# Optimization experiments

Measured on AMD Instinct MI355X. Metric: run time of the kernel, lower is better.

The kernel has to match this reference:

```python
import jax, jax.numpy as jnp
import numpy as np
from jax import lax

EPS = 1e-5
K = 3
PAD = 1
N_LAYERS = 7


def _conv2d(x, w, b):
    # x: [B,Cin,H,W], w: [Cout,Cin,K,K] -> [B,Cout,H,W], padding=1, stride=1
    y = lax.conv_general_dilated(x, w, window_strides=(1, 1),
                                 padding=[(PAD, PAD), (PAD, PAD)],
                                 dimension_numbers=('NCHW', 'OIHW', 'NCHW'))
    return y + b[None, :, None, None]


def _deform_conv2d(x, offset, weight):
    # torchvision deform_conv2d v1 (no mask, no bias), padding=PAD, stride=1.
    B, Cin, H, W = x.shape
    Cout = weight.shape[0]
    KK = K * K
    off = offset.reshape(B, KK, 2, H, W)
    dy = off[:, :, 0]  # [B,KK,H,W]
    dx = off[:, :, 1]
    kh = (jnp.arange(KK) // K).astype(x.dtype)  # row-major kernel taps
    kw = (jnp.arange(KK) % K).astype(x.dtype)
    hg = jnp.arange(H, dtype=x.dtype)
    wg = jnp.arange(W, dtype=x.dtype)
    # sampling positions p = p0 - pad + pk + offset
    py = dy + (hg[:, None] - PAD)[None, None, :, :] + kh[None, :, None, None]
    px = dx + (wg[None, :] - PAD)[None, None, :, :] + kw[None, :, None, None]
    y0 = jnp.floor(py)
    x0 = jnp.floor(px)
    ly = py - y0
    lx = px - x0
    y0i = y0.astype(jnp.int32)
    x0i = x0.astype(jnp.int32)

    def gather(img, yy, xx):  # img [Cin,H,W], yy/xx [KK,H,W]
        return img[:, yy, xx]  # [Cin,KK,H,W]

    gather_b = jax.vmap(gather)

    def corner(yi, xi, wgt):
        valid = (yi >= 0) & (yi < H) & (xi >= 0) & (xi < W)
        yc = jnp.clip(yi, 0, H - 1)
        xc = jnp.clip(xi, 0, W - 1)
        vals = gather_b(x, yc, xc)  # [B,Cin,KK,H,W]
        return vals * (wgt * valid)[:, None]

    sampled = (corner(y0i, x0i, (1 - ly) * (1 - lx))
               + corner(y0i, x0i + 1, (1 - ly) * lx)
               + corner(y0i + 1, x0i, ly * (1 - lx))
               + corner(y0i + 1, x0i + 1, ly * lx))  # [B,Cin,KK,H,W]
    return jnp.einsum('bikhw,oik->bohw', sampled, weight.reshape(Cout, Cin, KK))


def _layer(x, ow, ob, dw, g, b):
    offset = _conv2d(x, ow, ob)
    y = _deform_conv2d(x, offset, dw)
    # BatchNorm2d, training mode (batch stats, biased variance)
    mean = y.mean(axis=(0, 2, 3))
    var = y.var(axis=(0, 2, 3))
    yn = (y - mean[None, :, None, None]) * lax.rsqrt(var + EPS)[None, :, None, None]
    return jax.nn.relu(g[None, :, None, None] * yn + b[None, :, None, None])


def setup_inputs() -> dict:
    key = jax.random.key(0)
    ks = jax.random.split(key, 4)
    B, C, H, W = 4, 64, 128, 128
    x = jax.random.normal(ks[0], (B, C, H, W), dtype=jnp.float32)
    offset_w = jax.random.normal(ks[1], (N_LAYERS, 2 * K * K, C, K, K), dtype=jnp.float32) * 0.02
    offset_b = jnp.zeros((N_LAYERS, 2 * K * K), dtype=jnp.float32)
    deform_w = jax.random.normal(ks[2], (N_LAYERS, C, C, K, K), dtype=jnp.float32) * 0.05
    gamma = jnp.ones((N_LAYERS, C), dtype=jnp.float32)
    beta = jnp.zeros((N_LAYERS, C), dtype=jnp.float32)
    return {"x": x, "offset_w": offset_w, "offset_b": offset_b,
            "deform_w": deform_w, "gamma": gamma, "beta": beta}


def reference(x, offset_w, offset_b, deform_w, gamma, beta):
    def L(i, t):
        return _layer(t, offset_w[i], offset_b[i], deform_w[i], gamma[i], beta[i])
    # layer index map: 0=1_1, 1=1_2, 2=1_3, 3=1_4, 4=2_1, 5=2_2, 6=3
    out_1 = L(1, L(0, x))
    out_2 = L(4, x)
    out_sum_1 = out_1 + out_2
    out_1 = L(3, L(2, out_sum_1))
    out_2 = L(5, out_sum_1)
    out_3 = L(6, out_sum_1)
    return out_1 + out_2 + out_3
```

## Files before the change

kernel.cpp:

```cpp
#include <hip/hip_runtime.h>
#include <hip/hip_bf16.h>
#include <hip/hip_fp16.h>

#define NTOT 4194304
typedef __attribute__((ext_vector_type(4)))  short short4v;
typedef __attribute__((ext_vector_type(8)))  short short8v;
typedef __attribute__((ext_vector_type(4)))  float f32x4;
typedef __attribute__((ext_vector_type(2)))  float fx2;
typedef __attribute__((ext_vector_type(4)))  unsigned int uint4v;

__device__ __forceinline__ ushort f2bf(float f){
    __hip_bfloat16 h = __float2bfloat16(f);
    return __bfloat16_as_ushort(h);
}
__device__ __forceinline__ float bf2f(ushort u){
    return __uint_as_float(((unsigned)u)<<16);
}

__global__ __launch_bounds__(256) void pack_w(
    const float* __restrict__ dw, const float* __restrict__ ow,
    ushort* __restrict__ dwPk, ushort* __restrict__ owPk,
    float* __restrict__ statsG)
{
    int i = blockIdx.x*256 + threadIdx.x;
    if (i < 286720) {
        int j = i&3, co = (i>>2)&63, jg=(i>>8)&1, cih=(i>>9)&1, koff=(i>>10)&1;
        int r = i>>11; int kkp = r%5; int r2 = r/5; int ciq = r2&3; int l = r2>>2;
        int kk = kkp*2+koff, ci = ciq*16 + cih*8 + jg*4 + j;
        float v = (kk<9)? dw[((l*64+co)*64+ci)*9+kk] : 0.f;
        dwPk[i] = f2bf(v);
    }
    if (i < 143360) {
        int j = i&3, co = (i>>2)&31, jg=(i>>7)&1, cih=(i>>8)&1, koff=(i>>9)&1;
        int r = i>>10; int kkp = r%5; int r2 = r/5; int ciq = r2&3; int l = r2>>2;
        int kk = kkp*2+koff, ci = ciq*16 + cih*8 + jg*4 + j;
        float v = (kk<9 && co<18)? ow[((l*18+co)*64+ci)*9+kk] : 0.f;
        owPk[i] = f2bf(v);
    }
    if (i < 7*1024) statsG[i] = 0.f;
}

__global__ __launch_bounds__(256) void transpose_x(
    const float* __restrict__ src, ushort* __restrict__ xT)
{
    __shared__ ushort lds[128*72];
    const int bid = blockIdx.x, t = threadIdx.x;
    const int b = bid>>7, y = bid&127;
    const float* sp = src + (b<<20) + (y<<7);
#pragma unroll
    for (int i=0;i<32;i++){
        int lin = i*256 + t;
        int ci = lin>>7, xx = lin&127;
        lds[xx*72 + ci] = f2bf(sp[(ci<<14) + xx]);
    }
    __syncthreads();
    ushort* dp = xT + (((b<<7)+y)<<13);
#pragma unroll
    for (int i=0;i<4;i++){
        int u = i*256 + t;
        int xx = u>>3, cg = u&7;
        short8v v8 = *(const short8v*)(lds + xx*72 + cg*8);
        *(short8v*)(dp + (xx<<6) + cg*8) = v8;
    }
}

__constant__ int KHt[10] = {0,0,0,1,1,1,2,2,2,2};
__constant__ int KWt[10] = {0,1,2,0,1,2,0,1,2,2};

template<int NP>
__global__ __attribute__((amdgpu_flat_work_group_size(512,512), amdgpu_waves_per_eu(4,8)))
void dcn_layer(
    const ushort* __restrict__ xT, const ushort* __restrict__ owPkB,
    const float* __restrict__ obB, const ushort* __restrict__ dwPkB,
    ushort* __restrict__ ybB, float* __restrict__ statsB,
    int l0, int l1, int l2)
{
    constexpr int RS   = (NP==2)? 80 : 48;
    constexpr int UPP  = (NP==2)? 4  : 2;
    constexpr int SPS  = (NP==2)? 2  : 1;
    constexpr int CPP  = 4/NP;
    constexpr int TILE = 864*RS;
    constexpr int TOTU = 864*UPP;
    constexpr int ITER = (TOTU+511)/512;
    __shared__ __align__(16) char smem[TILE + 10240];
    __half* offh = (__half*)(smem + TILE);

    const int t = threadIdx.x, lane = t&63, w = t>>6;
    const int l15 = lane&15, lg = lane>>4;
    const int cih = lg&1, koff = lane>>5;
    const int bid = blockIdx.x;
    const int lsel = bid >> 8;
    const int tb = bid & 255;
    const int L = (lsel==0)? l0 : ((lsel==1)? l1 : l2);
    const ushort* owPk = owPkB + L*20480;
    const float*  ob   = obB   + L*18;
    const ushort* dwPk = dwPkB + L*40960;
    ushort* yb         = ybB + (size_t)lsel*NTOT;
    float*  statsL     = statsB + L*1024;

    const int xcd = tb&7, idx = tb>>3;
    const int b = xcd>>1, vh = xcd&1;
    const int ht = vh*8 + (idx>>2), wt = idx&3;
    const int w0 = wt*32, h0 = ht*8;
    const int row = h0 + w;
    const int RLO = h0-5, CLO = w0-8;
    const ushort* xb = xT + (b<<20);

    const short8v zz8 = (short8v){0,0,0,0,0,0,0,0};
    auto stage = [&](int P){
#pragma unroll 1
        for (int i=0;i<ITER;i++){
            int d = i*512 + t;
            if (d < TOTU) {
                int slot = d&(UPP-1), sp = d>>SPS;
                int rowt = sp/48, colt = sp - rowt*48;
                int gy = RLO+rowt, gx = CLO+colt;
                bool ok = ((unsigned)gy<128u) && ((unsigned)gx<128u);
                int gyc = min(max(gy,0),127), gxc = min(max(gx,0),127);
                short8v v = *(const short8v*)(xb + (((gyc<<7)+gxc)<<6) + (P*UPP+slot)*8);
                if (!ok) v = zz8;
                *(short8v*)(smem + sp*RS + ((slot^(sp&(UPP-1)))<<4)) = v;
            }
        }
    };

    f32x4 oacc[2][2];
#pragma unroll
    for (int p=0;p<2;p++)
#pragma unroll
        for (int q=0;q<2;q++) oacc[p][q] = (f32x4){0.f,0.f,0.f,0.f};

#pragma unroll 1
    for (int P=0; P<NP; ++P) {
        if (P) __syncthreads();
        stage(P);
        __syncthreads();
#pragma unroll 1
        for (int cil=0; cil<CPP; ++cil) {
            int ciq = P*CPP + cil;
            int unit = (NP==2)? ((cil<<1)|cih) : cih;
#pragma unroll 1
            for (int kkp=0; kkp<5; ++kkp) {
                int kkA = 2*kkp;
                int kkB = (kkA+1>8)?8:(kkA+1);
                int kh = koff ? KHt[kkB] : KHt[kkA];
                int kw = koff ? KWt[kkB] : KWt[kkA];
                short8v afr[2];
#pragma unroll
                for (int p=0;p<2;p++){
                    int rowt = w + kh + 4;
                    int colt = p*16 + l15 + kw + 7;
                    int sp = rowt*48 + colt;
                    afr[p] = *(const short8v*)(smem + sp*RS + ((unit^(sp&(UPP-1)))<<4));
                }
                const ushort* wop = owPk + ciq*5120 + kkp*1024 + koff*512 + cih*256;
#pragma unroll
                for (int q=0;q<2;q++){
                    short4v b0 = *(const short4v*)(wop +       (q*16+l15)*4);
                    short4v b1 = *(const short4v*)(wop + 128 + (q*16+l15)*4);
                    short8v bb = __builtin_shufflevector(b0,b1,0,1,2,3,4,5,6,7);
#pragma unroll
                    for (int p=0;p<2;p++)
                        oacc[p][q] = __builtin_amdgcn_mfma_f32_16x16x32_bf16(afr[p], bb, oacc[p][q], 0,0,0);
                }
            }
        }
    }

    {
        float biasq[2];
#pragma unroll
        for (int q=0;q<2;q++){ int o = q*16+l15; biasq[q] = (o<18)? ob[o] : 0.f; }
#pragma unroll
        for (int p=0;p<2;p++)
#pragma unroll
            for (int q=0;q<2;q++){
                int o = q*16+l15;
                if (o < 18) {
#pragma unroll
                    for (int r=0;r<4;r++){
                        int pix = w*32 + p*16 + lg*4 + r;
                        offh[pix*20 + o] = __float2half(oacc[p][q][r] + biasq[q]);
                    }
                }
            }
    }

    f32x4 acc[2][4];
#pragma unroll
    for (int p=0;p<2;p++)
#pragma unroll
        for (int q=0;q<4;q++) acc[p][q] = (f32x4){0.f,0.f,0.f,0.f};

#pragma unroll 1
    for (int P=0; P<NP; ++P) {
        __syncthreads();
        stage(P);
        __syncthreads();
#pragma unroll 1
        for (int cil=0; cil<CPP; ++cil) {
            int ciq = P*CPP + cil;
            int unit = (NP==2)? ((cil<<1)|cih) : cih;
#pragma unroll 1
            for (int kkp=0; kkp<5; ++kkp) {
                int kkA = 2*kkp;
                int kkB = (kkA+1>8)?8:(kkA+1);
                int kh = koff ? KHt[kkB] : KHt[kkA];
                int kw = koff ? KWt[kkB] : KWt[kkA];
                int kkX = koff ? kkB : kkA;
                short8v afr[2];
#pragma unroll
                for (int p=0;p<2;p++){
                    int pix = w*32 + p*16 + l15;
                    unsigned odp = *(const unsigned*)((const char*)offh + pix*40 + 4*kkX);
                    float dy = __half2float(__ushort_as_half((ushort)(odp & 0xffffu)));
                    float dx = __half2float(__ushort_as_half((ushort)(odp >> 16)));
                    float py = (float)(row + kh - 1) + dy;
                    float px = (float)(w0 + p*16 + l15 + kw - 1) + dx;
                    float fy = floorf(py), fx = floorf(px);
                    float ly = py - fy, lx = px - fx;
                    int y0 = (int)fy, x0 = (int)fx;
                    int y1 = y0+1, x1 = x0+1;
                    bool vy0 = ((unsigned)y0<128u), vy1 = ((unsigned)y1<128u);
                    bool vx0 = ((unsigned)x0<128u), vx1 = ((unsigned)x1<128u);
                    int y0c = min(max(y0,0),127), y1c = min(max(y1,0),127);
                    int x0c = min(max(x0,0),127), x1c = min(max(x1,0),127);
                    int r0 = y0c-RLO, r1 = y1c-RLO, c0 = x0c-CLO, c1 = x1c-CLO;
                    bool ty0 = ((unsigned)r0<18u), ty1 = ((unsigned)r1<18u);
                    bool tx0 = ((unsigned)c0<48u), tx1 = ((unsigned)c1<48u);
                    float g00 = (vy0&&vx0) ? (1.f-ly)*(1.f-lx) : 0.f;
                    float g01 = (vy0&&vx1) ? (1.f-ly)*lx       : 0.f;
                    float g10 = (vy1&&vx0) ? ly*(1.f-lx)       : 0.f;
                    float g11 = (vy1&&vx1) ? ly*lx             : 0.f;
                    float f00 = (ty0&&tx0) ? g00 : 0.f;
                    float f01 = (ty0&&tx1) ? g01 : 0.f;
                    float f10 = (ty1&&tx0) ? g10 : 0.f;
                    float f11 = (ty1&&tx1) ? g11 : 0.f;
                    int rc0 = min(max(r0,0),17), rc1 = min(max(r1,0),17);
                    int xc0 = min(max(c0,0),47), xc1 = min(max(c1,0),47);
                    int s00 = rc0*48+xc0, s01 = rc0*48+xc1, s10 = rc1*48+xc0, s11 = rc1*48+xc1;
                    uint4v q00 = *(const uint4v*)(smem + s00*RS + ((unit^(s00&(UPP-1)))<<4));
                    uint4v q01 = *(const uint4v*)(smem + s01*RS + ((unit^(s01&(UPP-1)))<<4));
                    uint4v q10 = *(const uint4v*)(smem + s10*RS + ((unit^(s10&(UPP-1)))<<4));
                    uint4v q11 = *(const uint4v*)(smem + s11*RS + ((unit^(s11&(UPP-1)))<<4));
                    fx2 F00 = {f00,f00}, F01 = {f01,f01}, F10 = {f10,f10}, F11 = {f11,f11};
                    fx2 sv2[4];
#pragma unroll
                    for (int k=0;k<4;k++){
                        fx2 xa = {__uint_as_float(q00[k]<<16), __uint_as_float(q00[k]&0xffff0000u)};
                        fx2 xb2= {__uint_as_float(q01[k]<<16), __uint_as_float(q01[k]&0xffff0000u)};
                        fx2 xc = {__uint_as_float(q10[k]<<16), __uint_as_float(q10[k]&0xffff0000u)};
                        fx2 xd = {__uint_as_float(q11[k]<<16), __uint_as_float(q11[k]&0xffff0000u)};
                        sv2[k] = xa*F00 + xb2*F01 + xc*F10 + xd*F11;
                    }
                    float r00 = g00-f00, r01 = g01-f01, r10 = g10-f10, r11 = g11-f11;
                    if (r00+r01+r10+r11 > 0.f) {
                        int cofs = (ciq*2 + cih)*8;
                        short8v a0 = *(const short8v*)(xb + ((((y0c<<7)+x0c)<<6) + cofs));
                        short8v a1 = *(const short8v*)(xb + ((((y0c<<7)+x1c)<<6) + cofs));
                        short8v a2 = *(const short8v*)(xb + ((((y1c<<7)+x0c)<<6) + cofs));
                        short8v a3 = *(const short8v*)(xb + ((((y1c<<7)+x1c)<<6) + cofs));
#pragma unroll
                        for (int j=0;j<8;j++){
                            float add = r00*bf2f((ushort)a0[j]) + r01*bf2f((ushort)a1[j])
                                      + r10*bf2f((ushort)a2[j]) + r11*bf2f((ushort)a3[j]);
                            if (j&1) sv2[j>>1].y += add; else sv2[j>>1].x += add;
                        }
                    }
#pragma unroll
                    for (int k=0;k<4;k++){
                        afr[p][2*k]   = (short)f2bf(sv2[k].x);
                        afr[p][2*k+1] = (short)f2bf(sv2[k].y);
                    }
                }
                const ushort* wp = dwPk + ciq*10240 + kkp*2048 + koff*1024 + cih*512;
#pragma unroll
                for (int q=0;q<4;q++){
                    short4v b0 = *(const short4v*)(wp +       (q*16+l15)*4);
                    short4v b1 = *(const short4v*)(wp + 256 + (q*16+l15)*4);
                    short8v bb = __builtin_shufflevector(b0,b1,0,1,2,3,4,5,6,7);
                    acc[0][q] = __builtin_amdgcn_mfma_f32_16x16x32_bf16(afr[0], bb, acc[0][q], 0,0,0);
                    acc[1][q] = __builtin_amdgcn_mfma_f32_16x16x32_bf16(afr[1], bb, acc[1][q], 0,0,0);
                }
            }
        }
    }

    float* yt  = (float*)smem;
    float* red = (float*)(smem + 33280);
#pragma unroll
    for (int half=0; half<2; ++half){
        __syncthreads();
#pragma unroll
        for (int p=0;p<2;p++)
#pragma unroll
            for (int qq=0;qq<2;qq++)
                *(f32x4*)(yt + (qq*16+l15)*260 + w*32 + p*16 + lg*4) = acc[p][half*2+qq];
        __syncthreads();
#pragma unroll
        for (int i=0;i<2;i++){
            int u = i*512 + t;
            int co = u>>5, px8 = (u&31)*8;
            short8v v8;
#pragma unroll
            for (int e=0;e<8;e++) v8[e] = (short)f2bf(yt[co*260 + px8 + e]);
            *(short8v*)(yb + ((((b<<6) + half*32 + co)<<14)
                        + ((h0 + (px8>>5))<<7) + w0 + (px8&31))) = v8;
        }
        {
            float s=0.f, s2=0.f;
            int co = t&31, seg = t>>5;
            const float* bp = yt + co*260 + seg*16;
#pragma unroll
            for (int qd=0;qd<16;qd++){ float v = bp[qd]; s += v; s2 += v*v; }
            red[seg*32+co] = s; red[512 + seg*32+co] = s2;
        }
        __syncthreads();
        if (t < 64){
            int vv = t>>5, cc = t&31;
            float a = 0.f;
#pragma unroll
            for (int g=0;g<16;g++) a += red[vv*512 + g*32 + cc];
            atomicAdd(statsL + (tb&7)*128 + vv*64 + half*32 + cc, a);
        }
    }
}

__global__ __launch_bounds__(256) void norm_fuse(
    const ushort* __restrict__ yv, const float* __restrict__ statsL,
    const float* __restrict__ gamma, const float* __restrict__ beta,
    const ushort* __restrict__ addB, float* __restrict__ dstF,
    ushort* __restrict__ dstB, ushort* __restrict__ xTout, int mode)
{
    __shared__ float scs[64], shs[64];
    __shared__ ushort lt[128*72];
    const int bid = blockIdx.x, t = threadIdx.x;
    const int b = bid>>7, y = bid&127;
    if (t < 64){
        float sum=0.f, ssq=0.f;
#pragma unroll
        for (int s=0;s<8;s++){ sum += statsL[s*128+t]; ssq += statsL[s*128+64+t]; }
        float mean = sum*(1.f/65536.f);
        float var  = ssq*(1.f/65536.f) - mean*mean;
        float inv  = rsqrtf(var + 1e-5f);
        float sc = gamma[t]*inv;
        scs[t] = sc; shs[t] = beta[t] - mean*sc;
    }
    __syncthreads();
#pragma unroll
    for (int i=0;i<4;i++){
        int g = i*256 + t;
        int ch = g>>4, xg = (g&15)*8;
        long base = (long)(((b<<6)+ch)<<14) + (y<<7) + xg;
        short8v v8 = *(const short8v*)(yv + base);
        float sc = scs[ch], sh = shs[ch];
        float r[8];
#pragma unroll
        for (int e=0;e<8;e++) r[e] = fmaxf(bf2f((ushort)v8[e])*sc+sh, 0.f);
        if (mode & 2) {
            short8v a8 = *(const short8v*)(addB + base);
#pragma unroll
            for (int e=0;e<8;e++) r[e] += bf2f((ushort)a8[e]);
        }
        if (mode & 4) {
            const float4* op = (const float4*)(dstF + base);
            float4 a0 = op[0], a1 = op[1];
            r[0]+=a0.x; r[1]+=a0.y; r[2]+=a0.z; r[3]+=a0.w;
            r[4]+=a1.x; r[5]+=a1.y; r[6]+=a1.z; r[7]+=a1.w;
        }
        if (mode & 5) {
            float4* dp = (float4*)(dstF + base);
            dp[0] = make_float4(r[0],r[1],r[2],r[3]);
            dp[1] = make_float4(r[4],r[5],r[6],r[7]);
        }
        if (mode & 16) {
            short8v o8;
#pragma unroll
            for (int e=0;e<8;e++) o8[e] = (short)f2bf(r[e]);
            *(short8v*)(dstB + base) = o8;
        }
        if (mode & 8) {
#pragma unroll
            for (int e=0;e<8;e++) lt[(xg+e)*72 + ch] = f2bf(r[e]);
        }
    }
    if (mode & 8) {
        __syncthreads();
        ushort* dp = xTout + (((b<<7)+y)<<13);
#pragma unroll
        for (int i=0;i<4;i++){
            int u = i*256 + t;
            int xx = u>>3, cg = u&7;
            short8v v8 = *(const short8v*)(lt + xx*72 + cg*8);
            *(short8v*)(dp + (xx<<6) + cg*8) = v8;
        }
    }
}

extern "C" void kernel_launch(void* const* d_in, const int* in_sizes, int n_in,
                              void* d_out, int out_size, void* d_ws, size_t ws_size,
                              hipStream_t stream)
{
    const float* x  = (const float*)d_in[0];
    const float* ow = (const float*)d_in[1];
    const float* ob = (const float*)d_in[2];
    const float* dw = (const float*)d_in[3];
    const float* g  = (const float*)d_in[4];
    const float* be = (const float*)d_in[5];
    float* out = (float*)d_out;

    ushort* yb     = (ushort*)d_ws;
    ushort* t4b    = yb + 3*(size_t)NTOT;
    ushort* xA     = t4b + NTOT;
    ushort* xB     = xA + NTOT;
    float*  statsG = (float*)(xB + NTOT);
    ushort* dwPk   = (ushort*)(statsG + 7*1024);
    ushort* owPk   = dwPk + 286720;

    pack_w<<<1120, 256, 0, stream>>>(dw, ow, dwPk, owPk, statsG);
    transpose_x<<<512, 256, 0, stream>>>(x, xA);

    auto nf = [&](int l, const ushort* ybp, int mode, const ushort* addB,
                  float* dstF, ushort* dstB, ushort* xout){
        norm_fuse<<<512, 256, 0, stream>>>(ybp, statsG + l*1024, g + l*64, be + l*64,
                                           addB, dstF, dstB, xout, mode);
    };

    dcn_layer<2><<<512, 512, 0, stream>>>(xA, owPk, ob, dwPk, yb, statsG, 4, 0, 4);
    nf(4, yb,        16, nullptr, nullptr, t4b,    nullptr);
    nf(0, yb+NTOT,    8, nullptr, nullptr, nullptr, xB);
    dcn_layer<2><<<256, 512, 0, stream>>>(xB, owPk, ob, dwPk, yb, statsG, 1, 1, 1);
    nf(1, yb,        10, t4b,    nullptr, nullptr, xA);
    dcn_layer<4><<<768, 512, 0, stream>>>(xA, owPk, ob, dwPk, yb, statsG, 2, 5, 6);
    nf(2, yb,         8, nullptr, nullptr, nullptr, xB);
    nf(5, yb+NTOT,    1, nullptr, out,     nullptr, nullptr);
    nf(6, yb+2*(size_t)NTOT, 5, nullptr, out, nullptr, nullptr);
    dcn_layer<2><<<256, 512, 0, stream>>>(xB, owPk, ob, dwPk, yb, statsG, 3, 3, 3);
    nf(3, yb,         5, nullptr, out,     nullptr, nullptr);
}
```

Before: 318.0 us.

## Pair layer 6 with layer 3 launch and drop NP=4 variant, simplify fallback

Removes the NP=4 template path and pairs layers differently: layer 2 runs with layer 5, and layer 6 now launches together with layer 3, reading a second input tensor. Each launch is 512 blocks using the larger tile layout. The bilinear gather drops the global-bounds clamp in the common path and takes the slow global-memory fallback only when a tap falls outside the staged tile but inside the image. This rebalances grid sizes across launches, removes the large 768-block launch, and trims per-sample ALU work. It also cuts the workspace to two y buffers. Layer 6's normalization moves to the end, and since both layers of the final launch now write through the two y buffers, correctness depends on that buffer indexing.

```diff
diff --git a/kernel.cpp b/kernel.cpp
--- a/kernel.cpp
+++ b/kernel.cpp
@@ -67,23 +67,15 @@
 __constant__ int KHt[10] = {0,0,0,1,1,1,2,2,2,2};
 __constant__ int KWt[10] = {0,1,2,0,1,2,0,1,2,2};
 
-template<int NP>
 __global__ __attribute__((amdgpu_flat_work_group_size(512,512), amdgpu_waves_per_eu(4,8)))
 void dcn_layer(
-    const ushort* __restrict__ xT, const ushort* __restrict__ owPkB,
-    const float* __restrict__ obB, const ushort* __restrict__ dwPkB,
-    ushort* __restrict__ ybB, float* __restrict__ statsB,
-    int l0, int l1, int l2)
+    const ushort* __restrict__ xTA, const ushort* __restrict__ xTB,
+    const ushort* __restrict__ owPkB, const float* __restrict__ obB,
+    const ushort* __restrict__ dwPkB, ushort* __restrict__ ybB,
+    float* __restrict__ statsB, int l0, int l1)
 {
-    constexpr int RS   = (NP==2)? 80 : 48;
-    constexpr int UPP  = (NP==2)? 4  : 2;
-    constexpr int SPS  = (NP==2)? 2  : 1;
-    constexpr int CPP  = 4/NP;
-    constexpr int TILE = 864*RS;
-    constexpr int TOTU = 864*UPP;
-    constexpr int ITER = (TOTU+511)/512;
-    __shared__ __align__(16) char smem[TILE + 10240];
-    __half* offh = (__half*)(smem + TILE);
+    __shared__ __align__(16) char smem[79360];
+    __half* offh = (__half*)(smem + 69120);
 
     const int t = threadIdx.x, lane = t&63, w = t>>6;
     const int l15 = lane&15, lg = lane>>4;
@@ -91,7 +83,7 @@
     const int bid = blockIdx.x;
     const int lsel = bid >> 8;
     const int tb = bid & 255;
-    const int L = (lsel==0)? l0 : ((lsel==1)? l1 : l2);
+    const int L = lsel ? l1 : l0;
     const ushort* owPk = owPkB + L*20480;
     const float*  ob   = obB   + L*18;
     const ushort* dwPk = dwPkB + L*40960;
@@ -104,22 +96,22 @@
     const int w0 = wt*32, h0 = ht*8;
     const int row = h0 + w;
     const int RLO = h0-5, CLO = w0-8;
-    const ushort* xb = xT + (b<<20);
+    const ushort* xb = (lsel ? xTB : xTA) + (b<<20);
 
     const short8v zz8 = (short8v){0,0,0,0,0,0,0,0};
     auto stage = [&](int P){
 #pragma unroll 1
-        for (int i=0;i<ITER;i++){
+        for (int i=0;i<7;i++){
             int d = i*512 + t;
-            if (d < TOTU) {
-                int slot = d&(UPP-1), sp = d>>SPS;
+            if (d < 3456) {
+                int slot = d&3, sp = d>>2;
                 int rowt = sp/48, colt = sp - rowt*48;
                 int gy = RLO+rowt, gx = CLO+colt;
                 bool ok = ((unsigned)gy<128u) && ((unsigned)gx<128u);
                 int gyc = min(max(gy,0),127), gxc = min(max(gx,0),127);
-                short8v v = *(const short8v*)(xb + (((gyc<<7)+gxc)<<6) + (P*UPP+slot)*8);
+                short8v v = *(const short8v*)(xb + (((gyc<<7)+gxc)<<6) + (P*4+slot)*8);
                 if (!ok) v = zz8;
-                *(short8v*)(smem + sp*RS + ((slot^(sp&(UPP-1)))<<4)) = v;
+                *(short8v*)(smem + sp*80 + ((slot^(sp&3))<<4)) = v;
             }
         }
     };
@@ -131,14 +123,14 @@
         for (int q=0;q<2;q++) oacc[p][q] = (f32x4){0.f,0.f,0.f,0.f};
 
 #pragma unroll 1
-    for (int P=0; P<NP; ++P) {
+    for (int P=0; P<2; ++P) {
         if (P) __syncthreads();
         stage(P);
         __syncthreads();
 #pragma unroll 1
-        for (int cil=0; cil<CPP; ++cil) {
-            int ciq = P*CPP + cil;
-            int unit = (NP==2)? ((cil<<1)|cih) : cih;
+        for (int cil=0; cil<2; ++cil) {
+            int ciq = P*2 + cil;
+            int unit = (cil<<1)|cih;
 #pragma unroll 1
             for (int kkp=0; kkp<5; ++kkp) {
                 int kkA = 2*kkp;
@@ -151,7 +143,7 @@
                     int rowt = w + kh + 4;
                     int colt = p*16 + l15 + kw + 7;
                     int sp = rowt*48 + colt;
-                    afr[p] = *(const short8v*)(smem + sp*RS + ((unit^(sp&(UPP-1)))<<4));
+                    afr[p] = *(const short8v*)(smem + sp*80 + ((unit^(sp&3))<<4));
                 }
                 const ushort* wop = owPk + ciq*5120 + kkp*1024 + koff*512 + cih*256;
 #pragma unroll
@@ -193,14 +185,14 @@
         for (int q=0;q<4;q++) acc[p][q] = (f32x4){0.f,0.f,0.f,0.f};
 
 #pragma unroll 1
-    for (int P=0; P<NP; ++P) {
+    for (int P=0; P<2; ++P) {
         __syncthreads();
         stage(P);
         __syncthreads();
 #pragma unroll 1
-        for (int cil=0; cil<CPP; ++cil) {
-            int ciq = P*CPP + cil;
-            int unit = (NP==2)? ((cil<<1)|cih) : cih;
+        for (int cil=0; cil<2; ++cil) {
+            int ciq = P*2 + cil;
+            int unit = (cil<<1)|cih;
 #pragma unroll 1
             for (int kkp=0; kkp<5; ++kkp) {
                 int kkA = 2*kkp;
@@ -220,29 +212,23 @@
                     float fy = floorf(py), fx = floorf(px);
                     float ly = py - fy, lx = px - fx;
                     int y0 = (int)fy, x0 = (int)fx;
-                    int y1 = y0+1, x1 = x0+1;
-                    bool vy0 = ((unsigned)y0<128u), vy1 = ((unsigned)y1<128u);
-                    bool vx0 = ((unsigned)x0<128u), vx1 = ((unsigned)x1<128u);
-                    int y0c = min(max(y0,0),127), y1c = min(max(y1,0),127);
-                    int x0c = min(max(x0,0),127), x1c = min(max(x1,0),127);
-                    int r0 = y0c-RLO, r1 = y1c-RLO, c0 = x0c-CLO, c1 = x1c-CLO;
+                    int r0 = y0 - RLO, c0 = x0 - CLO;
+                    int r1 = r0 + 1,  c1 = c0 + 1;
                     bool ty0 = ((unsigned)r0<18u), ty1 = ((unsigned)r1<18u);
                     bool tx0 = ((unsigned)c0<48u), tx1 = ((unsigned)c1<48u);
-                    float g00 = (vy0&&vx0) ? (1.f-ly)*(1.f-lx) : 0.f;
-                    float g01 = (vy0&&vx1) ? (1.f-ly)*lx       : 0.f;
-                    float g10 = (vy1&&vx0) ? ly*(1.f-lx)       : 0.f;
-                    float g11 = (vy1&&vx1) ? ly*lx             : 0.f;
-                    float f00 = (ty0&&tx0) ? g00 : 0.f;
-                    float f01 = (ty0&&tx1) ? g01 : 0.f;
-                    float f10 = (ty1&&tx0) ? g10 : 0.f;
-                    float f11 = (ty1&&tx1) ? g11 : 0.f;
+                    float w00 = (1.f-ly)*(1.f-lx), w01 = (1.f-ly)*lx;
+                    float w10 = ly*(1.f-lx),       w11 = ly*lx;
+                    float f00 = (ty0&&tx0)? w00 : 0.f;
+                    float f01 = (ty0&&tx1)? w01 : 0.f;
+                    float f10 = (ty1&&tx0)? w10 : 0.f;
+                    float f11 = (ty1&&tx1)? w11 : 0.f;
                     int rc0 = min(max(r0,0),17), rc1 = min(max(r1,0),17);
                     int xc0 = min(max(c0,0),47), xc1 = min(max(c1,0),47);
                     int s00 = rc0*48+xc0, s01 = rc0*48+xc1, s10 = rc1*48+xc0, s11 = rc1*48+xc1;
-                    uint4v q00 = *(const uint4v*)(smem + s00*RS + ((unit^(s00&(UPP-1)))<<4));
-                    uint4v q01 = *(const uint4v*)(smem + s01*RS + ((unit^(s01&(UPP-1)))<<4));
-                    uint4v q10 = *(const uint4v*)(smem + s10*RS + ((unit^(s10&(UPP-1)))<<4));
-                    uint4v q11 = *(const uint4v*)(smem + s11*RS + ((unit^(s11&(UPP-1)))<<4));
+                    uint4v q00 = *(const uint4v*)(smem + s00*80 + ((unit^(s00&3))<<4));
+                    uint4v q01 = *(const uint4v*)(smem + s01*80 + ((unit^(s01&3))<<4));
+                    uint4v q10 = *(const uint4v*)(smem + s10*80 + ((unit^(s10&3))<<4));
+                    uint4v q11 = *(const uint4v*)(smem + s11*80 + ((unit^(s11&3))<<4));
                     fx2 F00 = {f00,f00}, F01 = {f01,f01}, F10 = {f10,f10}, F11 = {f11,f11};
                     fx2 sv2[4];
 #pragma unroll
@@ -253,8 +239,18 @@
                         fx2 xd = {__uint_as_float(q11[k]<<16), __uint_as_float(q11[k]&0xffff0000u)};
                         sv2[k] = xa*F00 + xb2*F01 + xc*F10 + xd*F11;
                     }
-                    float r00 = g00-f00, r01 = g01-f01, r10 = g10-f10, r11 = g11-f11;
-                    if (r00+r01+r10+r11 > 0.f) {
+                    bool allIn = ty0 && ty1 && tx0 && tx1;
+                    bool inY = (y0 >= -1) && (y0 <= 127);
+                    bool inX = (x0 >= -1) && (x0 <= 127);
+                    if (__builtin_expect(!allIn && inY && inX, 0)) {
+                        bool vy0 = ((unsigned)y0<128u), vy1 = ((unsigned)(y0+1)<128u);
+                        bool vx0 = ((unsigned)x0<128u), vx1 = ((unsigned)(x0+1)<128u);
+                        float rw00 = (vy0&&vx0&&!(ty0&&tx0))? w00 : 0.f;
+                        float rw01 = (vy0&&vx1&&!(ty0&&tx1))? w01 : 0.f;
+                        float rw10 = (vy1&&vx0&&!(ty1&&tx0))? w10 : 0.f;
+                        float rw11 = (vy1&&vx1&&!(ty1&&tx1))? w11 : 0.f;
+                        int y0c=min(max(y0,0),127), y1c=min(max(y0+1,0),127);
+                        int x0c=min(max(x0,0),127), x1c=min(max(x0+1,0),127);
                         int cofs = (ciq*2 + cih)*8;
                         short8v a0 = *(const short8v*)(xb + ((((y0c<<7)+x0c)<<6) + cofs));
                         short8v a1 = *(const short8v*)(xb + ((((y0c<<7)+x1c)<<6) + cofs));
@@ -262,8 +258,8 @@
                         short8v a3 = *(const short8v*)(xb + ((((y1c<<7)+x1c)<<6) + cofs));
 #pragma unroll
                         for (int j=0;j<8;j++){
-                            float add = r00*bf2f((ushort)a0[j]) + r01*bf2f((ushort)a1[j])
-                                      + r10*bf2f((ushort)a2[j]) + r11*bf2f((ushort)a3[j]);
+                            float add = rw00*bf2f((ushort)a0[j]) + rw01*bf2f((ushort)a1[j])
+                                      + rw10*bf2f((ushort)a2[j]) + rw11*bf2f((ushort)a3[j]);
                             if (j&1) sv2[j>>1].y += add; else sv2[j>>1].x += add;
                         }
                     }
@@ -410,7 +406,7 @@
     float* out = (float*)d_out;
 
     ushort* yb     = (ushort*)d_ws;
-    ushort* t4b    = yb + 3*(size_t)NTOT;
+    ushort* t4b    = yb + 2*(size_t)NTOT;
     ushort* xA     = t4b + NTOT;
     ushort* xB     = xA + NTOT;
     float*  statsG = (float*)(xB + NTOT);
@@ -426,15 +422,15 @@
                                            addB, dstF, dstB, xout, mode);
     };
 
-    dcn_layer<2><<<512, 512, 0, stream>>>(xA, owPk, ob, dwPk, yb, statsG, 4, 0, 4);
+    dcn_layer<<<512, 512, 0, stream>>>(xA, xA, owPk, ob, dwPk, yb, statsG, 4, 0);
     nf(4, yb,        16, nullptr, nullptr, t4b,    nullptr);
     nf(0, yb+NTOT,    8, nullptr, nullptr, nullptr, xB);
-    dcn_layer<2><<<256, 512, 0, stream>>>(xB, owPk, ob, dwPk, yb, statsG, 1, 1, 1);
+    dcn_layer<<<256, 512, 0, stream>>>(xB, xB, owPk, ob, dwPk, yb, statsG, 1, 1);
     nf(1, yb,        10, t4b,    nullptr, nullptr, xA);
-    dcn_layer<4><<<768, 512, 0, stream>>>(xA, owPk, ob, dwPk, yb, statsG, 2, 5, 6);
+    dcn_layer<<<512, 512, 0, stream>>>(xA, xA, owPk, ob, dwPk, yb, statsG, 2, 5);
     nf(2, yb,         8, nullptr, nullptr, nullptr, xB);
     nf(5, yb+NTOT,    1, nullptr, out,     nullptr, nullptr);
-    nf(6, yb+2*(size_t)NTOT, 5, nullptr, out, nullptr, nullptr);
-    dcn_layer<2><<<256, 512, 0, stream>>>(xB, owPk, ob, dwPk, yb, statsG, 3, 3, 3);
+    dcn_layer<<<512, 512, 0, stream>>>(xB, xA, owPk, ob, dwPk, yb, statsG, 3, 6);
     nf(3, yb,         5, nullptr, out,     nullptr, nullptr);
-}
+    nf(6, yb+NTOT,    5, nullptr, out,     nullptr, nullptr);
+}
```

New measurement: 295.4 us. -7.1%, faster.
